# Performance work log

Hardware: AMD Instinct MI355X
Metric: run time of the kernel (lower is better)

The kernel has to match this reference:

```python
import jax, jax.numpy as jnp
import numpy as np

B, S, H, C = 4, 2048, 4, 64
D = H * C            # qDim = kDim = vDim = outDim = 256
WIN = 10             # localWindowSize


def setup_inputs() -> dict:
    key = jax.random.key(0)
    ks = jax.random.split(key, 10)
    f32 = jnp.float32
    inv = 1.0 / np.sqrt(D)
    return {
        "Qin": jax.random.normal(ks[0], (B, S, D), f32),
        "Kin": jax.random.normal(ks[1], (B, S, D), f32),
        "Vin": jax.random.normal(ks[2], (B, S, D), f32),
        "QTrans": jax.random.normal(ks[3], (D, H * C), f32) * inv,
        "KTrans": jax.random.normal(ks[4], (D, H * C), f32) * inv,
        "VTrans": jax.random.normal(ks[5], (D, H * C), f32) * inv,
        "GW": jax.random.normal(ks[6], (D, H * C), f32) * 0.02,
        "GB": jnp.ones((H * C,), f32),
        "OW": jax.random.normal(ks[7], (H * C, D), f32) * inv,
        "OB": jnp.zeros((D,), f32),
        "seqMask": jnp.zeros((B, S), dtype=bool),
    }


def reference(Qin, Kin, Vin, QTrans, KTrans, VTrans, GW, GB, OW, OB, seqMask):
    b, s = Qin.shape[0], Qin.shape[1]

    def heads(x, Wm):  # [b,s,D] @ [D,H*C] -> [H,b,s,C]
        return (x @ Wm).reshape(b, s, H, C).transpose(2, 0, 1, 3)

    Q = heads(Qin, QTrans)
    K = heads(Kin, KTrans)
    V = heads(Vin, VTrans)
    G = jax.nn.sigmoid((Vin @ GW + GB).reshape(b, s, H, C).transpose(2, 0, 1, 3))

    A = jnp.einsum('hnsi,hnti->hnst', Q, K) / jnp.sqrt(jnp.float32(C))
    idx = jnp.arange(s)
    band = jnp.abs(idx[:, None] - idx[None, :]) <= WIN          # [s,s]
    keep = band[None, None, :, :] & (~seqMask)[None, :, None, :]  # [1|H, b, s, s]
    A = jnp.where(keep, A, -jnp.inf)
    A = jax.nn.softmax(A, axis=-1)

    out = jnp.einsum('hnst,hnti,hnsi->nshi', A, V, G).reshape(b, s, H * C)
    return out @ OW + OB
```

## Files before the change

### kernel.cpp

```cpp
#include <hip/hip_runtime.h>
#include <hip/hip_bf16.h>
#include <math.h>

#define S_LEN 2048
#define NBATCH 4
#define DMODEL 256
#define NHEAD 4
#define HDIM 64
#define WINSZ 10
#define NROWS (NBATCH * S_LEN)
#define NT (2 * WINSZ + 1)
#define QB2 16
#define WR2 (QB2 + 2 * WINSZ)

typedef __attribute__((ext_vector_type(8))) short bf16x8;
typedef __attribute__((ext_vector_type(4))) float f32x4;

static __device__ __forceinline__ unsigned short f2bf(float f) {
    union { __hip_bfloat16 b; unsigned short u; } cv;
    cv.b = __float2bfloat16(f);
    return cv.u;
}
static __device__ __forceinline__ float bf2f(unsigned short s) {
    return __uint_as_float(((unsigned)s) << 16);
}

__global__ __launch_bounds__(256) void convert_weights(
    const float* __restrict__ QT, const float* __restrict__ KT,
    const float* __restrict__ VT, const float* __restrict__ GW,
    const float* __restrict__ OW, unsigned short* __restrict__ Wt)
{
    const int z = blockIdx.z;
    const float* src = (z == 0) ? QT : (z == 1) ? KT : (z == 2) ? VT
                       : (z == 3) ? GW : OW;
    unsigned short* dst = Wt + (size_t)z * DMODEL * DMODEL;

    __shared__ float tile[32][33];
    const int k0 = blockIdx.x * 32;
    const int n0 = blockIdx.y * 32;
    const int t = threadIdx.x;

    {
        const int kr = t >> 3;
        const int nc = (t & 7) * 4;
        const float4 v = *(const float4*)&src[(size_t)(k0 + kr) * DMODEL + n0 + nc];
        tile[kr][nc + 0] = v.x; tile[kr][nc + 1] = v.y;
        tile[kr][nc + 2] = v.z; tile[kr][nc + 3] = v.w;
    }
    __syncthreads();
    {
        const int nr = t >> 3;
        const int kc = (t & 7) * 4;
        unsigned short u[4];
#pragma unroll
        for (int j = 0; j < 4; ++j) u[j] = f2bf(tile[kc + j][nr]);
        *(ushort4*)&dst[(size_t)(n0 + nr) * DMODEL + k0 + kc] =
            *(const ushort4*)u;
    }
}

__global__ __launch_bounds__(256) void proj_kernel(
    const float* __restrict__ Qin, const float* __restrict__ Kin,
    const float* __restrict__ Vin, const unsigned short* __restrict__ Wt,
    const float* __restrict__ GB, unsigned short* __restrict__ Pout)
{
    __shared__ __align__(16) unsigned short As[128 * 64];
    __shared__ __align__(16) unsigned short Bs[64 * 64];

    const int z = blockIdx.z;
    const float* __restrict__ A = (z == 0) ? Qin : (z == 1) ? Kin : Vin;
    const unsigned short* __restrict__ W = Wt + (size_t)z * DMODEL * DMODEL;
    unsigned short* __restrict__ O = Pout + (size_t)z * NROWS * DMODEL;

    const int r0 = blockIdx.x * 128;
    const int c0 = blockIdx.y * 64;
    const int tid = threadIdx.x;
    const int lane = tid & 63;
    const int wid = tid >> 6;
    const int wr = wid >> 1;
    const int wc = wid & 1;
    const int lrow = lane & 15;
    const int lk = lane >> 4;

    f32x4 acc[4][2] = {};
    const uint4* Bg = (const uint4*)W;

    for (int kc = 0; kc < 256; kc += 64) {
#pragma unroll
        for (int p = 0; p < 4; ++p) {
            const int idx = p * 256 + tid;
            const int row = idx >> 3;
            const int ch = idx & 7;
            const float* src = A + (size_t)(r0 + row) * DMODEL + kc + ch * 8;
            const float4 f0 = *(const float4*)src;
            const float4 f1 = *(const float4*)(src + 4);
            unsigned short u[8] = {f2bf(f0.x), f2bf(f0.y), f2bf(f0.z), f2bf(f0.w),
                                   f2bf(f1.x), f2bf(f1.y), f2bf(f1.z), f2bf(f1.w)};
            ((uint4*)As)[row * 8 + (ch ^ (row & 7))] = *(const uint4*)u;
        }
        const int kq = kc >> 3;
#pragma unroll
        for (int p = 0; p < 2; ++p) {
            const int idx = p * 256 + tid;
            const int row = idx >> 3;
            const int ch = idx & 7;
            const uint4 v = Bg[(size_t)(c0 + row) * 32 + kq + ch];
            ((uint4*)Bs)[row * 8 + (ch ^ (row & 7))] = v;
        }
        __syncthreads();

#pragma unroll
        for (int kk = 0; kk < 2; ++kk) {
            const int chunk = kk * 4 + lk;
            bf16x8 a[4], b[2];
#pragma unroll
            for (int m = 0; m < 4; ++m) {
                const int row = wr * 64 + m * 16 + lrow;
                a[m] = ((const bf16x8*)As)[row * 8 + (chunk ^ (row & 7))];
            }
#pragma unroll
            for (int n = 0; n < 2; ++n) {
                const int row = wc * 32 + n * 16 + lrow;
                b[n] = ((const bf16x8*)Bs)[row * 8 + (chunk ^ (row & 7))];
            }
#pragma unroll
            for (int m = 0; m < 4; ++m)
#pragma unroll
                for (int n = 0; n < 2; ++n)
                    acc[m][n] = __builtin_amdgcn_mfma_f32_16x16x32_bf16(
                        a[m], b[n], acc[m][n], 0, 0, 0);
        }
        __syncthreads();
    }

    const bool sig = (z == 3);
#pragma unroll
    for (int m = 0; m < 4; ++m) {
#pragma unroll
        for (int n = 0; n < 2; ++n) {
            const int col = c0 + wc * 32 + n * 16 + lrow;
            const float bv = sig ? GB[col] : 0.0f;
#pragma unroll
            for (int reg = 0; reg < 4; ++reg) {
                const int row = r0 + wr * 64 + m * 16 + lk * 4 + reg;
                float v = acc[m][n][reg] + bv;
                if (sig) v = 1.0f / (1.0f + __expf(-v));
                O[(size_t)row * DMODEL + col] = f2bf(v);
            }
        }
    }
}

__global__ __launch_bounds__(256) void attn_outproj(
    const unsigned short* __restrict__ Qp, const unsigned short* __restrict__ Kp,
    const unsigned short* __restrict__ Vp, const unsigned short* __restrict__ Gp,
    const unsigned short* __restrict__ OWt, const float* __restrict__ OB,
    float* __restrict__ O)
{
    const int s0 = blockIdx.x * QB2;
    const int n = blockIdx.y;
    const int tid = threadIdx.x;

    __shared__ __align__(16) unsigned short sQ[QB2 * DMODEL];
    __shared__ __align__(16) unsigned short sK[WR2 * DMODEL];
    __shared__ __align__(16) unsigned short sV[WR2 * DMODEL];
    __shared__ __align__(16) unsigned short sAG[QB2 * DMODEL];
    __shared__ float sS[NHEAD][QB2][NT];

    const size_t base = (size_t)n * S_LEN;

    {
        const uint4* Qg = (const uint4*)Qp;
#pragma unroll
        for (int p = 0; p < 2; ++p) {
            const int idx = p * 256 + tid;
            const int q = idx >> 5, c = idx & 31;
            ((uint4*)sQ)[q * 32 + (c ^ (q & 7))] = Qg[(base + s0 + q) * 32 + c];
        }
        const uint4* Kg = (const uint4*)Kp;
        const uint4* Vg = (const uint4*)Vp;
#pragma unroll
        for (int p = 0; p < 9; ++p) {
            const int idx = p * 256 + tid;
            const int isV = idx >= WR2 * 32;
            const int rem = isV ? idx - WR2 * 32 : idx;
            const int r = rem >> 5, c = rem & 31;
            const int gs = min(max(s0 - WINSZ + r, 0), S_LEN - 1);
            const uint4 v = (isV ? Vg : Kg)[(base + gs) * 32 + c];
            ((uint4*)(isV ? sV : sK))[r * 32 + (c ^ (r & 7))] = v;
        }
    }
    __syncthreads();

#pragma unroll
    for (int p = 0; p < 6; ++p) {
        const int idx = p * 256 + tid;
        if (idx < QB2 * NHEAD * NT) {
            const int q = idx / (NHEAD * NT);
            const int rem = idx - q * (NHEAD * NT);
            const int h = rem / NT;
            const int i = rem - h * NT;
            const int r = q + i;
            float a0 = 0.f, a1 = 0.f;
#pragma unroll
            for (int j = 0; j < 8; ++j) {
                const bf16x8 kv = ((const bf16x8*)sK)[r * 32 + ((h * 8 + j) ^ (r & 7))];
                const bf16x8 qv = ((const bf16x8*)sQ)[q * 32 + ((h * 8 + j) ^ (q & 7))];
                float t0 = 0.f, t1 = 0.f;
#pragma unroll
                for (int e = 0; e < 4; ++e) {
                    t0 = fmaf(bf2f((unsigned short)kv[e]),
                              bf2f((unsigned short)qv[e]), t0);
                    t1 = fmaf(bf2f((unsigned short)kv[e + 4]),
                              bf2f((unsigned short)qv[e + 4]), t1);
                }
                a0 += t0; a1 += t1;
            }
            const int t = s0 + q - WINSZ + i;
            sS[h][q][i] = ((unsigned)t < (unsigned)S_LEN) ? (a0 + a1) * 0.125f
                                                          : -1e30f;
        }
    }
    __syncthreads();

#pragma unroll
    for (int p = 0; p < 2; ++p) {
        const int idx = p * 256 + tid;
        const int q = idx >> 5;
        const int h = (idx >> 3) & 3;
        const int cg = idx & 7;

        float pr[NT];
        float m = -1e30f;
#pragma unroll
        for (int i = 0; i < NT; ++i) { pr[i] = sS[h][q][i]; m = fmaxf(m, pr[i]); }
        float sum = 0.f;
#pragma unroll
        for (int i = 0; i < NT; ++i) { pr[i] = __expf(pr[i] - m); sum += pr[i]; }
        const float inv = 1.0f / sum;

        float acc[8] = {};
#pragma unroll
        for (int i = 0; i < NT; ++i) {
            const int r = q + i;
            const bf16x8 vv = ((const bf16x8*)sV)[r * 32 + ((h * 8 + cg) ^ (r & 7))];
#pragma unroll
            for (int j = 0; j < 8; ++j)
                acc[j] = fmaf(pr[i], bf2f((unsigned short)vv[j]), acc[j]);
        }
        const bf16x8 g8 = *(const bf16x8*)&Gp[(base + s0 + q) * DMODEL
                                             + h * HDIM + cg * 8];
        unsigned short outv[8];
#pragma unroll
        for (int j = 0; j < 8; ++j)
            outv[j] = f2bf(acc[j] * inv * bf2f((unsigned short)g8[j]));
        ((uint4*)sAG)[q * 32 + ((h * 8 + cg) ^ (q & 7))] = *(const uint4*)outv;
    }

    uint4* const BsBuf0 = (uint4*)sK;
    uint4* const BsBuf1 = (uint4*)sV;
    const uint4* Wg = (const uint4*)OWt;
    const int lane = tid & 63;
    const int w = tid >> 6;
    const int lrow = lane & 15;
    const int lk = lane >> 4;

#define STAGE_B(kc, dst)                                                     \
    {                                                                        \
        _Pragma("unroll")                                                    \
        for (int p = 0; p < 4; ++p) {                                        \
            const int idx = p * 256 + tid;                                   \
            const int nr = idx >> 2, c = idx & 3;                            \
            (dst)[nr * 4 + (c ^ (nr & 3))] = Wg[(size_t)nr * 32 + (kc) * 4 + c]; \
        }                                                                    \
    }

    STAGE_B(0, BsBuf0);
    __syncthreads();

    f32x4 acc4[4] = {};
#pragma unroll
    for (int kc = 0; kc < 8; ++kc) {
        if (kc < 7) {
            if ((kc & 1) == 0) STAGE_B(kc + 1, BsBuf1)
            else               STAGE_B(kc + 1, BsBuf0)
        }
        const uint4* cur = ((kc & 1) == 0) ? BsBuf0 : BsBuf1;
        const bf16x8 a =
            ((const bf16x8*)sAG)[lrow * 32 + ((kc * 4 + lk) ^ (lrow & 7))];
#pragma unroll
        for (int n4 = 0; n4 < 4; ++n4) {
            const int nr = w * 64 + n4 * 16 + lrow;
            const bf16x8 b = ((const bf16x8*)cur)[nr * 4 + (lk ^ (nr & 3))];
            acc4[n4] = __builtin_amdgcn_mfma_f32_16x16x32_bf16(a, b, acc4[n4],
                                                               0, 0, 0);
        }
        __syncthreads();
    }

#pragma unroll
    for (int n4 = 0; n4 < 4; ++n4) {
        const int col = w * 64 + n4 * 16 + lrow;
        const float bv = OB[col];
#pragma unroll
        for (int reg = 0; reg < 4; ++reg) {
            const int q = lk * 4 + reg;
            O[(base + s0 + q) * DMODEL + col] = acc4[n4][reg] + bv;
        }
    }
#undef STAGE_B
}

extern "C" void kernel_launch(void* const* d_in, const int* in_sizes, int n_in,
                              void* d_out, int out_size, void* d_ws, size_t ws_size,
                              hipStream_t stream)
{
    (void)in_sizes; (void)n_in; (void)out_size; (void)ws_size;

    const float* Qin = (const float*)d_in[0];
    const float* Kin = (const float*)d_in[1];
    const float* Vin = (const float*)d_in[2];
    const float* QT  = (const float*)d_in[3];
    const float* KT  = (const float*)d_in[4];
    const float* VT  = (const float*)d_in[5];
    const float* GW  = (const float*)d_in[6];
    const float* GB  = (const float*)d_in[7];
    const float* OW  = (const float*)d_in[8];
    const float* OB  = (const float*)d_in[9];

    float* out = (float*)d_out;

    const size_t NELEM = (size_t)NROWS * DMODEL;
    char* ws = (char*)d_ws;
    unsigned short* Wt = (unsigned short*)ws;
    unsigned short* Pp = (unsigned short*)(ws + 5 * DMODEL * DMODEL * 2);
    unsigned short* Qp = Pp;
    unsigned short* Kp = Pp + NELEM;
    unsigned short* Vp = Pp + 2 * NELEM;
    unsigned short* Gp = Pp + 3 * NELEM;
    unsigned short* OWt = Wt + (size_t)4 * DMODEL * DMODEL;

    convert_weights<<<dim3(8, 8, 5), 256, 0, stream>>>(QT, KT, VT, GW, OW, Wt);

    proj_kernel<<<dim3(NROWS / 128, DMODEL / 64, 4), 256, 0, stream>>>(
        Qin, Kin, Vin, Wt, GB, Pp);

    attn_outproj<<<dim3(S_LEN / QB2, NBATCH), 256, 0, stream>>>(
        Qp, Kp, Vp, Gp, OWt, OB, out);
}
```

Baseline: 42.68 us.

## Double-buffer shared-memory tiles in projection GEMM with register prefetch

Converts the projection kernel's K loop to a double-buffered pipeline. The next tile's global loads go into registers before the MFMA compute on the current LDS buffer, then get converted and written into the alternate buffer. This hides global load latency behind the matrix math and drops one barrier per iteration. In exchange it doubles LDS use (48KB per block) and raises register pressure, which may lower occupancy.

```diff
diff --git a/kernel.cpp b/kernel.cpp
--- a/kernel.cpp
+++ b/kernel.cpp
@@ -64,8 +64,8 @@
     const float* __restrict__ Vin, const unsigned short* __restrict__ Wt,
     const float* __restrict__ GB, unsigned short* __restrict__ Pout)
 {
-    __shared__ __align__(16) unsigned short As[128 * 64];
-    __shared__ __align__(16) unsigned short Bs[64 * 64];
+    __shared__ __align__(16) unsigned short As[2][128 * 64];
+    __shared__ __align__(16) unsigned short Bs[2][64 * 64];
 
     const int z = blockIdx.z;
     const float* __restrict__ A = (z == 0) ? Qin : (z == 1) ? Kin : Vin;
@@ -82,32 +82,59 @@
     const int lrow = lane & 15;
     const int lk = lane >> 4;
 
+    const uint4* Bg = (const uint4*)W;
+
+    const int arow = tid >> 3;
+    const int ach = tid & 7;
+    float4 fa0[4], fa1[4];
+    uint4 bv[2];
+
+#define LOAD_TILE(kc)                                                        \
+    {                                                                        \
+        _Pragma("unroll")                                                    \
+        for (int p = 0; p < 4; ++p) {                                        \
+            const float* src = A + (size_t)(r0 + arow + p * 32) * DMODEL     \
+                               + (kc) + ach * 8;                             \
+            fa0[p] = *(const float4*)src;                                    \
+            fa1[p] = *(const float4*)(src + 4);                              \
+        }                                                                    \
+        _Pragma("unroll")                                                    \
+        for (int p = 0; p < 2; ++p) {                                        \
+            const int idx = p * 256 + tid;                                   \
+            bv[p] = Bg[(size_t)(c0 + (idx >> 3)) * 32 + ((kc) >> 3)          \
+                       + (idx & 7)];                                         \
+        }                                                                    \
+    }
+
+#define WRITE_TILE(buf)                                                      \
+    {                                                                        \
+        _Pragma("unroll")                                                    \
+        for (int p = 0; p < 4; ++p) {                                        \
+            const int row = arow + p * 32;                                   \
+            unsigned short u[8] = {f2bf(fa0[p].x), f2bf(fa0[p].y),           \
+                                   f2bf(fa0[p].z), f2bf(fa0[p].w),           \
+                                   f2bf(fa1[p].x), f2bf(fa1[p].y),           \
+                                   f2bf(fa1[p].z), f2bf(fa1[p].w)};          \
+            ((uint4*)As[buf])[row * 8 + (ach ^ (row & 7))] = *(const uint4*)u;\
+        }                                                                    \
+        _Pragma("unroll")                                                    \
+        for (int p = 0; p < 2; ++p) {                                        \
+            const int idx = p * 256 + tid;                                   \
+            const int row = idx >> 3, ch = idx & 7;                          \
+            ((uint4*)Bs[buf])[row * 8 + (ch ^ (row & 7))] = bv[p];           \
+        }                                                                    \
+    }
+
     f32x4 acc[4][2] = {};
-    const uint4* Bg = (const uint4*)W;
-
-    for (int kc = 0; kc < 256; kc += 64) {
-#pragma unroll
-        for (int p = 0; p < 4; ++p) {
-            const int idx = p * 256 + tid;
-            const int row = idx >> 3;
-            const int ch = idx & 7;
-            const float* src = A + (size_t)(r0 + row) * DMODEL + kc + ch * 8;
-            const float4 f0 = *(const float4*)src;
-            const float4 f1 = *(const float4*)(src + 4);
-            unsigned short u[8] = {f2bf(f0.x), f2bf(f0.y), f2bf(f0.z), f2bf(f0.w),
-                                   f2bf(f1.x), f2bf(f1.y), f2bf(f1.z), f2bf(f1.w)};
-            ((uint4*)As)[row * 8 + (ch ^ (row & 7))] = *(const uint4*)u;
-        }
-        const int kq = kc >> 3;
-#pragma unroll
-        for (int p = 0; p < 2; ++p) {
-            const int idx = p * 256 + tid;
-            const int row = idx >> 3;
-            const int ch = idx & 7;
-            const uint4 v = Bg[(size_t)(c0 + row) * 32 + kq + ch];
-            ((uint4*)Bs)[row * 8 + (ch ^ (row & 7))] = v;
-        }
-        __syncthreads();
+
+    LOAD_TILE(0);
+    WRITE_TILE(0);
+    __syncthreads();
+
+#pragma unroll
+    for (int ki = 0; ki < 4; ++ki) {
+        const int cur = ki & 1;
+        if (ki < 3) LOAD_TILE((ki + 1) * 64);
 
 #pragma unroll
         for (int kk = 0; kk < 2; ++kk) {
@@ -116,12 +143,12 @@
 #pragma unroll
             for (int m = 0; m < 4; ++m) {
                 const int row = wr * 64 + m * 16 + lrow;
-                a[m] = ((const bf16x8*)As)[row * 8 + (chunk ^ (row & 7))];
+                a[m] = ((const bf16x8*)As[cur])[row * 8 + (chunk ^ (row & 7))];
             }
 #pragma unroll
             for (int n = 0; n < 2; ++n) {
                 const int row = wc * 32 + n * 16 + lrow;
-                b[n] = ((const bf16x8*)Bs)[row * 8 + (chunk ^ (row & 7))];
+                b[n] = ((const bf16x8*)Bs[cur])[row * 8 + (chunk ^ (row & 7))];
             }
 #pragma unroll
             for (int m = 0; m < 4; ++m)
@@ -130,8 +157,14 @@
                     acc[m][n] = __builtin_amdgcn_mfma_f32_16x16x32_bf16(
                         a[m], b[n], acc[m][n], 0, 0, 0);
         }
-        __syncthreads();
-    }
+
+        if (ki < 3) {
+            WRITE_TILE(cur ^ 1);
+            __syncthreads();
+        }
+    }
+#undef LOAD_TILE
+#undef WRITE_TILE
 
     const bool sig = (z == 3);
 #pragma unroll
@@ -139,11 +172,11 @@
 #pragma unroll
         for (int n = 0; n < 2; ++n) {
             const int col = c0 + wc * 32 + n * 16 + lrow;
-            const float bv = sig ? GB[col] : 0.0f;
+            const float bv2 = sig ? GB[col] : 0.0f;
 #pragma unroll
             for (int reg = 0; reg < 4; ++reg) {
                 const int row = r0 + wr * 64 + m * 16 + lk * 4 + reg;
-                float v = acc[m][n][reg] + bv;
+                float v = acc[m][n][reg] + bv2;
                 if (sig) v = 1.0f / (1.0f + __expf(-v));
                 O[(size_t)row * DMODEL + col] = f2bf(v);
             }
```

Measured after the change: 44.20 us. 3.5% more time.

## Fuse Q and gate projections into attention kernel, drop Q/G intermediates

Applied to the files above, without the earlier changes.

The Q projection and the sigmoid gate projection move out of the standalone projection kernel and into the attention kernel. Each attention block converts its 16 Qin and Vin rows to bf16 in shared memory and computes Q and G with MFMA, reading the transposed weights directly from global memory. This avoids writing and re-reading the Q and G intermediates (two NROWS x 256 bf16 tensors) and halves the projection grid. In exchange, the attention kernel gains extra MFMA work and uncached weight loads, plus more LDS, which may reduce occupancy.

```diff
diff --git a/kernel.cpp b/kernel.cpp
--- a/kernel.cpp
+++ b/kernel.cpp
@@ -12,6 +12,7 @@
 #define NT (2 * WINSZ + 1)
 #define QB2 16
 #define WR2 (QB2 + 2 * WINSZ)
+#define WSTRIDE (DMODEL * DMODEL)
 
 typedef __attribute__((ext_vector_type(8))) short bf16x8;
 typedef __attribute__((ext_vector_type(4))) float f32x4;
@@ -33,7 +34,7 @@
     const int z = blockIdx.z;
     const float* src = (z == 0) ? QT : (z == 1) ? KT : (z == 2) ? VT
                        : (z == 3) ? GW : OW;
-    unsigned short* dst = Wt + (size_t)z * DMODEL * DMODEL;
+    unsigned short* dst = Wt + (size_t)z * WSTRIDE;
 
     __shared__ float tile[32][33];
     const int k0 = blockIdx.x * 32;
@@ -59,18 +60,18 @@
     }
 }
 
-__global__ __launch_bounds__(256) void proj_kernel(
-    const float* __restrict__ Qin, const float* __restrict__ Kin,
-    const float* __restrict__ Vin, const unsigned short* __restrict__ Wt,
-    const float* __restrict__ GB, unsigned short* __restrict__ Pout)
+__global__ __launch_bounds__(256) void proj_kv(
+    const float* __restrict__ Kin, const float* __restrict__ Vin,
+    const unsigned short* __restrict__ Wt,
+    unsigned short* __restrict__ Kp, unsigned short* __restrict__ Vp)
 {
     __shared__ __align__(16) unsigned short As[128 * 64];
     __shared__ __align__(16) unsigned short Bs[64 * 64];
 
     const int z = blockIdx.z;
-    const float* __restrict__ A = (z == 0) ? Qin : (z == 1) ? Kin : Vin;
-    const unsigned short* __restrict__ W = Wt + (size_t)z * DMODEL * DMODEL;
-    unsigned short* __restrict__ O = Pout + (size_t)z * NROWS * DMODEL;
+    const float* __restrict__ A = (z == 0) ? Kin : Vin;
+    const unsigned short* __restrict__ W = Wt + (size_t)(z + 1) * WSTRIDE;
+    unsigned short* __restrict__ O = (z == 0) ? Kp : Vp;
 
     const int r0 = blockIdx.x * 128;
     const int c0 = blockIdx.y * 64;
@@ -133,49 +134,57 @@
         __syncthreads();
     }
 
-    const bool sig = (z == 3);
 #pragma unroll
     for (int m = 0; m < 4; ++m) {
 #pragma unroll
         for (int n = 0; n < 2; ++n) {
             const int col = c0 + wc * 32 + n * 16 + lrow;
-            const float bv = sig ? GB[col] : 0.0f;
 #pragma unroll
             for (int reg = 0; reg < 4; ++reg) {
                 const int row = r0 + wr * 64 + m * 16 + lk * 4 + reg;
-                float v = acc[m][n][reg] + bv;
-                if (sig) v = 1.0f / (1.0f + __expf(-v));
-                O[(size_t)row * DMODEL + col] = f2bf(v);
-            }
-        }
-    }
-}
-
-__global__ __launch_bounds__(256) void attn_outproj(
-    const unsigned short* __restrict__ Qp, const unsigned short* __restrict__ Kp,
-    const unsigned short* __restrict__ Vp, const unsigned short* __restrict__ Gp,
-    const unsigned short* __restrict__ OWt, const float* __restrict__ OB,
-    float* __restrict__ O)
+                O[(size_t)row * DMODEL + col] = f2bf(acc[m][n][reg]);
+            }
+        }
+    }
+}
+
+__global__ __launch_bounds__(256) void attn_fused(
+    const float* __restrict__ Qin, const float* __restrict__ Vin,
+    const unsigned short* __restrict__ Kp, const unsigned short* __restrict__ Vp,
+    const unsigned short* __restrict__ Wt, const float* __restrict__ GB,
+    const float* __restrict__ OB, float* __restrict__ O)
 {
     const int s0 = blockIdx.x * QB2;
     const int n = blockIdx.y;
     const int tid = threadIdx.x;
 
+    __shared__ __align__(16) unsigned short sA[32 * DMODEL];
     __shared__ __align__(16) unsigned short sQ[QB2 * DMODEL];
     __shared__ __align__(16) unsigned short sK[WR2 * DMODEL];
     __shared__ __align__(16) unsigned short sV[WR2 * DMODEL];
-    __shared__ __align__(16) unsigned short sAG[QB2 * DMODEL];
+    __shared__ __align__(16) unsigned short sG[QB2 * DMODEL];
     __shared__ float sS[NHEAD][QB2][NT];
+    unsigned short* const sAG = sA;
 
     const size_t base = (size_t)n * S_LEN;
+    const int lane = tid & 63;
+    const int w = tid >> 6;
+    const int lrow = lane & 15;
+    const int lk = lane >> 4;
 
     {
-        const uint4* Qg = (const uint4*)Qp;
-#pragma unroll
-        for (int p = 0; p < 2; ++p) {
+#pragma unroll
+        for (int p = 0; p < 4; ++p) {
             const int idx = p * 256 + tid;
-            const int q = idx >> 5, c = idx & 31;
-            ((uint4*)sQ)[q * 32 + (c ^ (q & 7))] = Qg[(base + s0 + q) * 32 + c];
+            const int r = idx >> 5, c = idx & 31;
+            const float* src = ((r < 16) ? Qin + (base + s0 + r) * DMODEL
+                                         : Vin + (base + s0 + r - 16) * DMODEL)
+                               + c * 8;
+            const float4 f0 = *(const float4*)src;
+            const float4 f1 = *(const float4*)(src + 4);
+            unsigned short u[8] = {f2bf(f0.x), f2bf(f0.y), f2bf(f0.z), f2bf(f0.w),
+                                   f2bf(f1.x), f2bf(f1.y), f2bf(f1.z), f2bf(f1.w)};
+            ((uint4*)sA)[r * 32 + (c ^ (r & 7))] = *(const uint4*)u;
         }
         const uint4* Kg = (const uint4*)Kp;
         const uint4* Vg = (const uint4*)Vp;
@@ -188,6 +197,42 @@
             const int gs = min(max(s0 - WINSZ + r, 0), S_LEN - 1);
             const uint4 v = (isV ? Vg : Kg)[(base + gs) * 32 + c];
             ((uint4*)(isV ? sV : sK))[r * 32 + (c ^ (r & 7))] = v;
+        }
+    }
+    __syncthreads();
+
+    {
+        const unsigned short* QTt = Wt;
+        const unsigned short* GWt = Wt + (size_t)3 * WSTRIDE;
+        f32x4 qacc[4] = {}, gacc[4] = {};
+#pragma unroll
+        for (int kk = 0; kk < 8; ++kk) {
+            const int chunk = kk * 4 + lk;
+            const bf16x8 aq = ((const bf16x8*)sA)[lrow * 32 + (chunk ^ (lrow & 7))];
+            const bf16x8 ag = ((const bf16x8*)sA)[(16 + lrow) * 32 + (chunk ^ (lrow & 7))];
+#pragma unroll
+            for (int nf = 0; nf < 4; ++nf) {
+                const int col = w * 64 + nf * 16 + lrow;
+                const bf16x8 bq = ((const bf16x8*)QTt)[(size_t)col * 32 + chunk];
+                const bf16x8 bg = ((const bf16x8*)GWt)[(size_t)col * 32 + chunk];
+                qacc[nf] = __builtin_amdgcn_mfma_f32_16x16x32_bf16(aq, bq, qacc[nf], 0, 0, 0);
+                gacc[nf] = __builtin_amdgcn_mfma_f32_16x16x32_bf16(ag, bg, gacc[nf], 0, 0, 0);
+            }
+        }
+#pragma unroll
+        for (int nf = 0; nf < 4; ++nf) {
+            const int col = w * 64 + nf * 16 + lrow;
+            const int cq = col >> 3, ce = col & 7;
+            const float gb = GB[col];
+#pragma unroll
+            for (int reg = 0; reg < 4; ++reg) {
+                const int row = lk * 4 + reg;
+                sQ[row * DMODEL + ((cq ^ (row & 7)) << 3) + ce] =
+                    f2bf(qacc[nf][reg]);
+                float gv = gacc[nf][reg] + gb;
+                gv = 1.0f / (1.0f + __expf(-gv));
+                sG[row * DMODEL + ((cq ^ (row & 7)) << 3) + ce] = f2bf(gv);
+            }
         }
     }
     __syncthreads();
@@ -248,8 +293,7 @@
             for (int j = 0; j < 8; ++j)
                 acc[j] = fmaf(pr[i], bf2f((unsigned short)vv[j]), acc[j]);
         }
-        const bf16x8 g8 = *(const bf16x8*)&Gp[(base + s0 + q) * DMODEL
-                                             + h * HDIM + cg * 8];
+        const bf16x8 g8 = ((const bf16x8*)sG)[q * 32 + ((h * 8 + cg) ^ (q & 7))];
         unsigned short outv[8];
 #pragma unroll
         for (int j = 0; j < 8; ++j)
@@ -259,11 +303,7 @@
 
     uint4* const BsBuf0 = (uint4*)sK;
     uint4* const BsBuf1 = (uint4*)sV;
-    const uint4* Wg = (const uint4*)OWt;
-    const int lane = tid & 63;
-    const int w = tid >> 6;
-    const int lrow = lane & 15;
-    const int lk = lane >> 4;
+    const uint4* Wg = (const uint4*)(Wt + (size_t)4 * WSTRIDE);
 
 #define STAGE_B(kc, dst)                                                     \
     {                                                                        \
@@ -333,18 +373,14 @@
     const size_t NELEM = (size_t)NROWS * DMODEL;
     char* ws = (char*)d_ws;
     unsigned short* Wt = (unsigned short*)ws;
-    unsigned short* Pp = (unsigned short*)(ws + 5 * DMODEL * DMODEL * 2);
-    unsigned short* Qp = Pp;
-    unsigned short* Kp = Pp + NELEM;
-    unsigned short* Vp = Pp + 2 * NELEM;
-    unsigned short* Gp = Pp + 3 * NELEM;
-    unsigned short* OWt = Wt + (size_t)4 * DMODEL * DMODEL;
+    unsigned short* Kp = (unsigned short*)(ws + 5 * WSTRIDE * 2);
+    unsigned short* Vp = Kp + NELEM;
 
     convert_weights<<<dim3(8, 8, 5), 256, 0, stream>>>(QT, KT, VT, GW, OW, Wt);
 
-    proj_kernel<<<dim3(NROWS / 128, DMODEL / 64, 4), 256, 0, stream>>>(
-        Qin, Kin, Vin, Wt, GB, Pp);
-
-    attn_outproj<<<dim3(S_LEN / QB2, NBATCH), 256, 0, stream>>>(
-        Qp, Kp, Vp, Gp, OWt, OB, out);
-}
+    proj_kv<<<dim3(NROWS / 128, DMODEL / 64, 2), 256, 0, stream>>>(
+        Kin, Vin, Wt, Kp, Vp);
+
+    attn_fused<<<dim3(S_LEN / QB2, NBATCH), 256, 0, stream>>>(
+        Qin, Vin, Kp, Vp, Wt, GB, OB, out);
+}
```

After: 55.59 us. 1.3x slower.
